# Optimization experiments

Measured on AMD Instinct MI355X. Metric: run time of the kernel, lower is better.

Reference implementation:

```python
import math
import jax
import jax.numpy as jnp
import numpy as np

N_NODE = 50000
N_EDGE = 1_600_000
D_IN = 128
D_K = 32
N_HEADS = 8


def setup_inputs() -> dict:
    key = jax.random.key(0)
    k_h, k_e, k_q, k_k, k_v = jax.random.split(key, 5)
    h = jax.random.normal(k_h, (N_NODE, D_IN), dtype=jnp.float32)
    edge_idx = jax.random.randint(k_e, (2, N_EDGE), 0, N_NODE, dtype=jnp.int64)
    scale = 1.0 / math.sqrt(D_IN)
    WQ = jax.random.normal(k_q, (N_HEADS, D_IN, D_K), dtype=jnp.float32) * scale
    WK = jax.random.normal(k_k, (N_HEADS, D_IN, D_K), dtype=jnp.float32) * scale
    WV = jax.random.normal(k_v, (N_HEADS, D_IN, D_K), dtype=jnp.float32) * scale
    return {"h": h, "edge_idx": edge_idx, "WQ": WQ, "WK": WK, "WV": WV}


def reference(h, edge_idx, WQ, WK, WV):
    n_node = h.shape[0]
    d_k = WK.shape[-1]
    # Per-head projections: [H, N, d]
    Q = jnp.einsum('nd,hdk->hnk', h, WQ)
    K = jnp.einsum('nd,hdk->hnk', h, WK)
    V = jnp.einsum('nd,hdv->hnv', h, WV)
    row = edge_idx[0]  # destination (softmax normalized per row, dim=1)
    col = edge_idx[1]  # source
    # Edge logits: e[h, e] = <Q[h, row[e]], K[h, col[e]]> / sqrt(d_k)
    e = jnp.einsum('hek,hek->he', Q[:, row, :], K[:, col, :]) / jnp.sqrt(
        jnp.asarray(d_k, dtype=h.dtype))
    eT = e.T  # [E, H]
    # Sparse (segment) softmax over outgoing edges of each row node.
    m = jax.ops.segment_max(eT, row, num_segments=n_node)  # [N, H]
    m = jnp.where(jnp.isfinite(m), m, jnp.zeros_like(m))   # guard empty rows
    ex = jnp.exp(eT - m[row])                               # [E, H]
    denom = jax.ops.segment_sum(ex, row, num_segments=n_node)  # [N, H]
    att = ex / denom[row]                                   # [E, H]
    # Sparse mm: out[i] = sum_{edges (i,j)} att * V[j]
    msgs = att[:, :, None] * jnp.transpose(V, (1, 0, 2))[col]  # [E, H, d_v]
    out = jax.ops.segment_sum(msgs, row, num_segments=n_node)  # [N, H, d_v]
    # aggregate == 'concat' -> head-major concat along feature dim
    return out.reshape(n_node, -1)
```

## Files before the change

kernel.cpp:

```cpp
#include <hip/hip_runtime.h>
#include <hip/hip_bf16.h>
#include <cstdint>

#define D_IN 128
#define DK 32
#define NH 8
#define HD 256

typedef __attribute__((ext_vector_type(8))) short short8;
typedef __attribute__((ext_vector_type(4))) float f32x4;

__device__ inline float u2f(unsigned int u) {
  union { unsigned int i; float f; } c; c.i = u; return c.f;
}
__device__ inline short f2bf(float f) {
  union { float f; unsigned int i; } c; c.f = f;
  unsigned int u = c.i;
  u = u + 0x7FFFu + ((u >> 16) & 1u);
  return (short)(u >> 16);
}

__global__ __launch_bounds__(256) void prep_w_kernel(
    const float* __restrict__ WQ, const float* __restrict__ WK,
    const float* __restrict__ WV, short8* __restrict__ Bbuf) {
  int ct = blockIdx.x;
  int t = threadIdx.x;
  int kt = t >> 6, L = t & 63;
  int col = ct * 16 + (L & 15);
  int type = col >> 8;
  const float* W = (type == 0) ? WQ : (type == 1) ? WK : WV;
  int head = (col & 255) >> 5;
  int kk = col & 31;
  int k0 = kt * 32 + ((L >> 4) << 3);
  short8 o;
  #pragma unroll
  for (int r = 0; r < 8; r++)
    o[r] = f2bf(W[head * (D_IN * DK) + (k0 + r) * DK + kk]);
  Bbuf[(size_t)(ct * 4 + kt) * 64 + L] = o;
}

__global__ __launch_bounds__(256) void gemm_qkv_kernel(
    const float* __restrict__ h, const short8* __restrict__ Bbuf,
    __hip_bfloat16* __restrict__ Qh, __hip_bfloat16* __restrict__ KVh,
    int nt_total, int n_node) {
  __shared__ float hs[16][132];
  __shared__ short lds[16][768];
  int nt = blockIdx.x;
  int t = threadIdx.x;
  {
    const float4* h4 = (const float4*)(h + (size_t)nt * 16 * 128);
    float4 v0 = h4[t * 2], v1 = h4[t * 2 + 1];
    int node = t >> 4, dim = (t & 15) * 8;
    hs[node][dim + 0] = v0.x; hs[node][dim + 1] = v0.y;
    hs[node][dim + 2] = v0.z; hs[node][dim + 3] = v0.w;
    hs[node][dim + 4] = v1.x; hs[node][dim + 5] = v1.y;
    hs[node][dim + 6] = v1.z; hs[node][dim + 7] = v1.w;
  }
  __syncthreads();
  int w = t >> 6;
  int L = t & 63;
  int arow = L & 15, k0base = ((L >> 4) << 3);
  short8 afrag[4];
  #pragma unroll
  for (int kt = 0; kt < 4; kt++) {
    #pragma unroll
    for (int r = 0; r < 8; r++)
      afrag[kt][r] = f2bf(hs[arow][kt * 32 + k0base + r]);
  }
  f32x4 acc[12];
  #pragma unroll
  for (int c = 0; c < 12; c++) acc[c] = (f32x4){0.f, 0.f, 0.f, 0.f};
  #pragma unroll
  for (int kt = 0; kt < 4; kt++) {
    #pragma unroll
    for (int c = 0; c < 12; c++) {
      short8 b = Bbuf[(size_t)((w * 12 + c) * 4 + kt) * 64 + L];
      acc[c] = __builtin_amdgcn_mfma_f32_16x16x32_bf16(afrag[kt], b, acc[c], 0, 0, 0);
    }
  }
  int row0 = (L >> 4) << 2;
  int col0 = w * 192 + (L & 15);
  #pragma unroll
  for (int c = 0; c < 12; c++) {
    #pragma unroll
    for (int r = 0; r < 4; r++)
      lds[row0 + r][col0 + c * 16] = f2bf(acc[c][r]);
  }
  __syncthreads();
  #pragma unroll
  for (int j = 0; j < 2; j++) {
    int u = t + j * 256;
    int hh = u >> 6, r2 = (u >> 2) & 15, part = u & 3;
    float4 vdat = *(const float4*)&lds[r2][hh * 32 + part * 8];
    *(float4*)(Qh + ((size_t)hh * n_node + nt * 16 + r2) * 32 + part * 8) = vdat;
  }
  #pragma unroll
  for (int j = 0; j < 4; j++) {
    int u = t + j * 256;
    int hh = u >> 7, r2 = (u >> 3) & 15, part = u & 7;
    int srccol = (part < 4) ? (256 + hh * 32 + part * 8)
                            : (512 + hh * 32 + (part - 4) * 8);
    float4 vdat = *(const float4*)&lds[r2][srccol];
    *(float4*)(KVh + ((size_t)hh * n_node + nt * 16 + r2) * 64 +
               ((part < 4) ? part * 8 : 32 + (part - 4) * 8)) = vdat;
  }
}

__global__ void rank_kernel(const int* __restrict__ row, int n_edge,
                            int* __restrict__ cnt, int* __restrict__ rank) {
  int i = blockIdx.x * blockDim.x + threadIdx.x;
  if (i < n_edge) rank[i] = atomicAdd(&cnt[row[i]], 1);
}

__global__ __launch_bounds__(256) void scan1_kernel(
    const int* __restrict__ cnt, int n, int* __restrict__ exc,
    int* __restrict__ bsum) {
  __shared__ int s[256];
  int gid = blockIdx.x * 256 + threadIdx.x;
  int v = (gid < n) ? cnt[gid] : 0;
  s[threadIdx.x] = v;
  __syncthreads();
  #pragma unroll
  for (int off = 1; off < 256; off <<= 1) {
    int t = (threadIdx.x >= off) ? s[threadIdx.x - off] : 0;
    __syncthreads();
    s[threadIdx.x] += t;
    __syncthreads();
  }
  if (gid < n) exc[gid] = s[threadIdx.x] - v;
  if (threadIdx.x == 255) bsum[blockIdx.x] = s[255];
}

__global__ __launch_bounds__(256) void scan2_kernel(int* __restrict__ bsum,
                                                    int nb) {
  __shared__ int s[256];
  int v = (threadIdx.x < nb) ? bsum[threadIdx.x] : 0;
  s[threadIdx.x] = v;
  __syncthreads();
  #pragma unroll
  for (int off = 1; off < 256; off <<= 1) {
    int t = (threadIdx.x >= off) ? s[threadIdx.x - off] : 0;
    __syncthreads();
    s[threadIdx.x] += t;
    __syncthreads();
  }
  if (threadIdx.x < nb) bsum[threadIdx.x] = s[threadIdx.x] - v;
}

__global__ __launch_bounds__(256) void scan3_kernel(
    int* __restrict__ exc, const int* __restrict__ bsum, int n, int n_edge) {
  int gid = blockIdx.x * 256 + threadIdx.x;
  if (gid < n) exc[gid] = exc[gid] + bsum[blockIdx.x];
  if (gid == 0) exc[n] = n_edge;
}

__global__ void scatter_kernel(const int* __restrict__ row,
                               const int* __restrict__ col,
                               const int* __restrict__ rank, int n_edge,
                               const int* __restrict__ offsets,
                               int* __restrict__ col_sorted) {
  int i = blockIdx.x * blockDim.x + threadIdx.x;
  if (i < n_edge) col_sorted[offsets[row[i]] + rank[i]] = col[i];
}

#define PROC(r, vld)                                                         \
  {                                                                          \
    float x0 = u2f(r.x << 16), x1 = u2f(r.x & 0xFFFF0000u);                  \
    float x2 = u2f(r.y << 16), x3 = u2f(r.y & 0xFFFF0000u);                  \
    float x4 = u2f(r.z << 16), x5 = u2f(r.z & 0xFFFF0000u);                  \
    float x6 = u2f(r.w << 16), x7 = u2f(r.w & 0xFFFF0000u);                  \
    float d = x0 * qf0;                                                      \
    d = fmaf(x1, qf1, d); d = fmaf(x2, qf2, d); d = fmaf(x3, qf3, d);        \
    d = fmaf(x4, qf4, d); d = fmaf(x5, qf5, d); d = fmaf(x6, qf6, d);        \
    d = fmaf(x7, qf7, d);                                                    \
    d += __shfl_xor(d, 1);                                                   \
    d += __shfl_xor(d, 2);                                                   \
    float tt = __shfl_xor(d, 4);                                             \
    float lg = (s < 4) ? d : tt;                                             \
    float p = (vld) ? __expf(lg) : 0.f;                                      \
    denom += p;                                                              \
    a0 = fmaf(p, x0, a0); a1 = fmaf(p, x1, a1);                              \
    a2 = fmaf(p, x2, a2); a3 = fmaf(p, x3, a3);                              \
    a4 = fmaf(p, x4, a4); a5 = fmaf(p, x5, a5);                              \
    a6 = fmaf(p, x6, a6); a7 = fmaf(p, x7, a7);                              \
  }

__global__ __launch_bounds__(256) void attn_kernel(
    const __hip_bfloat16* __restrict__ Qh, const __hip_bfloat16* __restrict__ KVh,
    const int* __restrict__ offsets, const int* __restrict__ col_sorted,
    float* __restrict__ out, int n_node) {
  int head = blockIdx.x & 7;
  int grp = blockIdx.x >> 3;
  int wave = threadIdx.x >> 6;
  int lane = threadIdx.x & 63;
  int g = lane >> 3;
  int s = lane & 7;
  int node = grp * 4 + wave;
  if (node >= n_node) return;
  int start = offsets[node], end = offsets[node + 1];

  if (end <= start) {
    if (g == 0 && s >= 4) {
      float* op = out + (size_t)node * HD + head * 32 + (s - 4) * 8;
      float4 z = make_float4(0.f, 0.f, 0.f, 0.f);
      *(float4*)op = z;
      *(float4*)(op + 4) = z;
    }
    return;
  }

  const float QS = 0.17677669529663687f;
  float qf0, qf1, qf2, qf3, qf4, qf5, qf6, qf7;
  {
    uint4 qr = *(const uint4*)((const char*)(Qh +
                ((size_t)head * n_node + node) * 32) + (s & 3) * 16);
    qf0 = u2f(qr.x << 16) * QS; qf1 = u2f(qr.x & 0xFFFF0000u) * QS;
    qf2 = u2f(qr.y << 16) * QS; qf3 = u2f(qr.y & 0xFFFF0000u) * QS;
    qf4 = u2f(qr.z << 16) * QS; qf5 = u2f(qr.z & 0xFFFF0000u) * QS;
    qf6 = u2f(qr.w << 16) * QS; qf7 = u2f(qr.w & 0xFFFF0000u) * QS;
  }
  float denom = 0.f;
  float a0 = 0.f, a1 = 0.f, a2 = 0.f, a3 = 0.f;
  float a4 = 0.f, a5 = 0.f, a6 = 0.f, a7 = 0.f;

  const char* kvb = (const char*)KVh + (size_t)head * n_node * 128 + s * 16;

  for (int base = start; base < end; base += 16) {
    int i0 = base + g, i1 = base + 8 + g;
    bool v0 = i0 < end, v1 = i1 < end;
    int c0 = col_sorted[v0 ? i0 : start];
    int c1 = col_sorted[v1 ? i1 : start];
    uint4 r0 = *(const uint4*)(kvb + (size_t)c0 * 128);
    uint4 r1 = *(const uint4*)(kvb + (size_t)c1 * 128);
    PROC(r0, v0);
    PROC(r1, v1);
  }

  denom += __shfl_xor(denom, 8); denom += __shfl_xor(denom, 16);
  denom += __shfl_xor(denom, 32);
  a0 += __shfl_xor(a0, 8); a0 += __shfl_xor(a0, 16); a0 += __shfl_xor(a0, 32);
  a1 += __shfl_xor(a1, 8); a1 += __shfl_xor(a1, 16); a1 += __shfl_xor(a1, 32);
  a2 += __shfl_xor(a2, 8); a2 += __shfl_xor(a2, 16); a2 += __shfl_xor(a2, 32);
  a3 += __shfl_xor(a3, 8); a3 += __shfl_xor(a3, 16); a3 += __shfl_xor(a3, 32);
  a4 += __shfl_xor(a4, 8); a4 += __shfl_xor(a4, 16); a4 += __shfl_xor(a4, 32);
  a5 += __shfl_xor(a5, 8); a5 += __shfl_xor(a5, 16); a5 += __shfl_xor(a5, 32);
  a6 += __shfl_xor(a6, 8); a6 += __shfl_xor(a6, 16); a6 += __shfl_xor(a6, 32);
  a7 += __shfl_xor(a7, 8); a7 += __shfl_xor(a7, 16); a7 += __shfl_xor(a7, 32);

  float inv = 1.f / denom;
  if (g == 0 && s >= 4) {
    float* op = out + (size_t)node * HD + head * 32 + (s - 4) * 8;
    float4 o0 = make_float4(a0 * inv, a1 * inv, a2 * inv, a3 * inv);
    float4 o1 = make_float4(a4 * inv, a5 * inv, a6 * inv, a7 * inv);
    *(float4*)op = o0;
    *(float4*)(op + 4) = o1;
  }
}

extern "C" void kernel_launch(void* const* d_in, const int* in_sizes, int n_in,
                              void* d_out, int out_size, void* d_ws,
                              size_t ws_size, hipStream_t stream) {
  const float* h = (const float*)d_in[0];
  const int* edge = (const int*)d_in[1];
  const float* WQ = (const float*)d_in[2];
  const float* WK = (const float*)d_in[3];
  const float* WV = (const float*)d_in[4];
  float* out = (float*)d_out;

  int n_node = in_sizes[0] / D_IN;
  int n_edge = in_sizes[1] / 2;
  const int* row = edge;
  const int* col = edge + n_edge;

  char* ws = (char*)d_ws;
  size_t off = 0;
  auto alloc = [&](size_t bytes) {
    void* p = ws + off;
    off += (bytes + 255) & ~(size_t)255;
    return p;
  };
  int nt_total = (n_node + 15) / 16;
  __hip_bfloat16* Qh = (__hip_bfloat16*)alloc((size_t)NH * n_node * 32 * 2);
  __hip_bfloat16* KVh = (__hip_bfloat16*)alloc((size_t)NH * n_node * 64 * 2);
  short8* Bbuf = (short8*)alloc((size_t)48 * 4 * 64 * 16);
  int* col_sorted = (int*)alloc((size_t)n_edge * 4);
  int* rank = (int*)alloc((size_t)n_edge * 4);
  int* cnt = (int*)alloc((size_t)n_node * 4);
  int* offsets = (int*)alloc((size_t)(n_node + 1) * 4);
  int* bsum = (int*)alloc(256 * 4);

  hipMemsetAsync(cnt, 0, (size_t)n_node * 4, stream);

  prep_w_kernel<<<48, 256, 0, stream>>>(WQ, WK, WV, Bbuf);
  gemm_qkv_kernel<<<nt_total, 256, 0, stream>>>(h, Bbuf, Qh, KVh, nt_total,
                                                n_node);

  int nb_e = (n_edge + 255) / 256;
  rank_kernel<<<nb_e, 256, 0, stream>>>(row, n_edge, cnt, rank);

  int nb = (n_node + 255) / 256;
  scan1_kernel<<<nb, 256, 0, stream>>>(cnt, n_node, offsets, bsum);
  scan2_kernel<<<1, 256, 0, stream>>>(bsum, nb);
  scan3_kernel<<<nb, 256, 0, stream>>>(offsets, bsum, n_node, n_edge);

  scatter_kernel<<<nb_e, 256, 0, stream>>>(row, col, rank, n_edge, offsets,
                                           col_sorted);

  attn_kernel<<<((n_node + 3) / 4) * 8, 256, 0, stream>>>(
      Qh, KVh, offsets, col_sorted, out, n_node);
}
```

Baseline: 368.4 us.

## Compute edge logits with MFMA and fold softmax scale into Q projection

The per-edge Q·K dot products in the attention kernel now come from a 16x16x32 bf16 MFMA over 16 gathered K rows, instead of scalar FMAs followed by shuffle reductions. The 1/sqrt(d_k)·log2(e) factor is applied to Q when it is written out in the projection kernel, so the attention loop can use exp2f directly. K and V gathers are split across lanes in a new layout, and the final reduction needs fewer shuffles. This removes shuffle and ALU work per edge, at the cost of separate K and V gathers per lane and a select to pick each lane's weight. The softmax still has no max subtraction, as before.

```diff
diff --git a/kernel.cpp b/kernel.cpp
--- a/kernel.cpp
+++ b/kernel.cpp
@@ -80,11 +80,13 @@
   }
   int row0 = (L >> 4) << 2;
   int col0 = w * 192 + (L & 15);
+  const float QSL = 0.25506966f;
   #pragma unroll
   for (int c = 0; c < 12; c++) {
+    float sc = ((w * 192 + c * 16) < 256) ? QSL : 1.f;
     #pragma unroll
     for (int r = 0; r < 4; r++)
-      lds[row0 + r][col0 + c * 16] = f2bf(acc[c][r]);
+      lds[row0 + r][col0 + c * 16] = f2bf(acc[c][r] * sc);
   }
   __syncthreads();
   #pragma unroll
@@ -163,45 +165,27 @@
   if (i < n_edge) col_sorted[offsets[row[i]] + rank[i]] = col[i];
 }
 
-#define PROC(r, vld)                                                         \
-  {                                                                          \
-    float x0 = u2f(r.x << 16), x1 = u2f(r.x & 0xFFFF0000u);                  \
-    float x2 = u2f(r.y << 16), x3 = u2f(r.y & 0xFFFF0000u);                  \
-    float x4 = u2f(r.z << 16), x5 = u2f(r.z & 0xFFFF0000u);                  \
-    float x6 = u2f(r.w << 16), x7 = u2f(r.w & 0xFFFF0000u);                  \
-    float d = x0 * qf0;                                                      \
-    d = fmaf(x1, qf1, d); d = fmaf(x2, qf2, d); d = fmaf(x3, qf3, d);        \
-    d = fmaf(x4, qf4, d); d = fmaf(x5, qf5, d); d = fmaf(x6, qf6, d);        \
-    d = fmaf(x7, qf7, d);                                                    \
-    d += __shfl_xor(d, 1);                                                   \
-    d += __shfl_xor(d, 2);                                                   \
-    float tt = __shfl_xor(d, 4);                                             \
-    float lg = (s < 4) ? d : tt;                                             \
-    float p = (vld) ? __expf(lg) : 0.f;                                      \
-    denom += p;                                                              \
-    a0 = fmaf(p, x0, a0); a1 = fmaf(p, x1, a1);                              \
-    a2 = fmaf(p, x2, a2); a3 = fmaf(p, x3, a3);                              \
-    a4 = fmaf(p, x4, a4); a5 = fmaf(p, x5, a5);                              \
-    a6 = fmaf(p, x6, a6); a7 = fmaf(p, x7, a7);                              \
-  }
-
 __global__ __launch_bounds__(256) void attn_kernel(
     const __hip_bfloat16* __restrict__ Qh, const __hip_bfloat16* __restrict__ KVh,
     const int* __restrict__ offsets, const int* __restrict__ col_sorted,
     float* __restrict__ out, int n_node) {
   int head = blockIdx.x & 7;
   int grp = blockIdx.x >> 3;
-  int wave = threadIdx.x >> 6;
+  int wv = threadIdx.x >> 6;
   int lane = threadIdx.x & 63;
-  int g = lane >> 3;
-  int s = lane & 7;
-  int node = grp * 4 + wave;
+  int node = grp * 4 + wv;
   if (node >= n_node) return;
   int start = offsets[node], end = offsets[node + 1];
 
+  int kc = lane >> 4;
+  int erow = lane & 15;
+  int vc = lane & 3;
+  int vchunk = (lane >> 2) & 3;
+  int vslot = (kc << 2) | vc;
+
   if (end <= start) {
-    if (g == 0 && s >= 4) {
-      float* op = out + (size_t)node * HD + head * 32 + (s - 4) * 8;
+    if (vc == 0 && kc == 0) {
+      float* op = out + (size_t)node * HD + head * 32 + vchunk * 8;
       float4 z = make_float4(0.f, 0.f, 0.f, 0.f);
       *(float4*)op = z;
       *(float4*)(op + 4) = z;
@@ -209,47 +193,48 @@
     return;
   }
 
-  const float QS = 0.17677669529663687f;
-  float qf0, qf1, qf2, qf3, qf4, qf5, qf6, qf7;
-  {
-    uint4 qr = *(const uint4*)((const char*)(Qh +
-                ((size_t)head * n_node + node) * 32) + (s & 3) * 16);
-    qf0 = u2f(qr.x << 16) * QS; qf1 = u2f(qr.x & 0xFFFF0000u) * QS;
-    qf2 = u2f(qr.y << 16) * QS; qf3 = u2f(qr.y & 0xFFFF0000u) * QS;
-    qf4 = u2f(qr.z << 16) * QS; qf5 = u2f(qr.z & 0xFFFF0000u) * QS;
-    qf6 = u2f(qr.w << 16) * QS; qf7 = u2f(qr.w & 0xFFFF0000u) * QS;
-  }
-  float denom = 0.f;
+  short8 qb = *(const short8*)(Qh + ((size_t)head * n_node + node) * 32 + kc * 8);
+
+  float dn = 0.f;
   float a0 = 0.f, a1 = 0.f, a2 = 0.f, a3 = 0.f;
   float a4 = 0.f, a5 = 0.f, a6 = 0.f, a7 = 0.f;
-
-  const char* kvb = (const char*)KVh + (size_t)head * n_node * 128 + s * 16;
+  const char* kvb = (const char*)KVh + (size_t)head * n_node * 128;
 
   for (int base = start; base < end; base += 16) {
-    int i0 = base + g, i1 = base + 8 + g;
-    bool v0 = i0 < end, v1 = i1 < end;
-    int c0 = col_sorted[v0 ? i0 : start];
-    int c1 = col_sorted[v1 ? i1 : start];
-    uint4 r0 = *(const uint4*)(kvb + (size_t)c0 * 128);
-    uint4 r1 = *(const uint4*)(kvb + (size_t)c1 * 128);
-    PROC(r0, v0);
-    PROC(r1, v1);
-  }
-
-  denom += __shfl_xor(denom, 8); denom += __shfl_xor(denom, 16);
-  denom += __shfl_xor(denom, 32);
-  a0 += __shfl_xor(a0, 8); a0 += __shfl_xor(a0, 16); a0 += __shfl_xor(a0, 32);
-  a1 += __shfl_xor(a1, 8); a1 += __shfl_xor(a1, 16); a1 += __shfl_xor(a1, 32);
-  a2 += __shfl_xor(a2, 8); a2 += __shfl_xor(a2, 16); a2 += __shfl_xor(a2, 32);
-  a3 += __shfl_xor(a3, 8); a3 += __shfl_xor(a3, 16); a3 += __shfl_xor(a3, 32);
-  a4 += __shfl_xor(a4, 8); a4 += __shfl_xor(a4, 16); a4 += __shfl_xor(a4, 32);
-  a5 += __shfl_xor(a5, 8); a5 += __shfl_xor(a5, 16); a5 += __shfl_xor(a5, 32);
-  a6 += __shfl_xor(a6, 8); a6 += __shfl_xor(a6, 16); a6 += __shfl_xor(a6, 32);
-  a7 += __shfl_xor(a7, 8); a7 += __shfl_xor(a7, 16); a7 += __shfl_xor(a7, 32);
-
-  float inv = 1.f / denom;
-  if (g == 0 && s >= 4) {
-    float* op = out + (size_t)node * HD + head * 32 + (s - 4) * 8;
+    int iK = base + erow;
+    int iV = base + vslot;
+    int cK = col_sorted[iK < end ? iK : start];
+    int cV = col_sorted[iV < end ? iV : start];
+    short8 kf = *(const short8*)(kvb + (size_t)cK * 128 + kc * 16);
+    uint4 vf = *(const uint4*)(kvb + (size_t)cV * 128 + 64 + vchunk * 16);
+    f32x4 dm = __builtin_amdgcn_mfma_f32_16x16x32_bf16(
+        kf, qb, (f32x4){0.f, 0.f, 0.f, 0.f}, 0, 0, 0);
+    int e0 = base + (kc << 2);
+    float p0 = (e0 < end) ? exp2f(dm[0]) : 0.f;
+    float p1 = (e0 + 1 < end) ? exp2f(dm[1]) : 0.f;
+    float p2 = (e0 + 2 < end) ? exp2f(dm[2]) : 0.f;
+    float p3 = (e0 + 3 < end) ? exp2f(dm[3]) : 0.f;
+    dn += (p0 + p1) + (p2 + p3);
+    float pb = (vc == 0) ? p0 : (vc == 1) ? p1 : (vc == 2) ? p2 : p3;
+    a0 = fmaf(pb, u2f(vf.x << 16), a0);
+    a1 = fmaf(pb, u2f(vf.x & 0xFFFF0000u), a1);
+    a2 = fmaf(pb, u2f(vf.y << 16), a2);
+    a3 = fmaf(pb, u2f(vf.y & 0xFFFF0000u), a3);
+    a4 = fmaf(pb, u2f(vf.z << 16), a4);
+    a5 = fmaf(pb, u2f(vf.z & 0xFFFF0000u), a5);
+    a6 = fmaf(pb, u2f(vf.w << 16), a6);
+    a7 = fmaf(pb, u2f(vf.w & 0xFFFF0000u), a7);
+  }
+
+#define RED4(x)                                                              \
+  x += __shfl_xor(x, 1); x += __shfl_xor(x, 2);                              \
+  x += __shfl_xor(x, 16); x += __shfl_xor(x, 32);
+  RED4(a0) RED4(a1) RED4(a2) RED4(a3) RED4(a4) RED4(a5) RED4(a6) RED4(a7)
+  dn += __shfl_xor(dn, 16);
+  dn += __shfl_xor(dn, 32);
+  float inv = 1.f / dn;
+  if (vc == 0 && kc == 0) {
+    float* op = out + (size_t)node * HD + head * 32 + vchunk * 8;
     float4 o0 = make_float4(a0 * inv, a1 * inv, a2 * inv, a3 * inv);
     float4 o1 = make_float4(a4 * inv, a5 * inv, a6 * inv, a7 * inv);
     *(float4*)op = o0;
```

Result: slower. 454.1 us (+23.3%).

## Pad CSR rows to multiples of 16 with a zero sentinel node, drop bounds checks

Applied to the files above, without the earlier changes.

Each node's edge segment is padded to a multiple of 16 and filled with a sentinel column that points to an extra all-zero K/V row. This removes the per-edge validity predicates in the attention loop. Each padded edge contributes exp(0)=1 to the denominator, which is subtracted using the true count. The Q scale is folded into the GEMM as 1/sqrt(d)*log2(e) so the loop can use exp2f. The cost is a fill kernel over the padded column array, a larger col_sorted buffer, and extra wasted gathers of the zero row. Like the original code, it skips the max subtraction and depends on the logits staying small.

```diff
diff --git a/kernel.cpp b/kernel.cpp
--- a/kernel.cpp
+++ b/kernel.cpp
@@ -80,11 +80,13 @@
   }
   int row0 = (L >> 4) << 2;
   int col0 = w * 192 + (L & 15);
+  const float QSL = 0.25506966f;
   #pragma unroll
   for (int c = 0; c < 12; c++) {
+    float sc = ((w * 192 + c * 16) < 256) ? QSL : 1.f;
     #pragma unroll
     for (int r = 0; r < 4; r++)
-      lds[row0 + r][col0 + c * 16] = f2bf(acc[c][r]);
+      lds[row0 + r][col0 + c * 16] = f2bf(acc[c][r] * sc);
   }
   __syncthreads();
   #pragma unroll
@@ -101,8 +103,18 @@
     int srccol = (part < 4) ? (256 + hh * 32 + part * 8)
                             : (512 + hh * 32 + (part - 4) * 8);
     float4 vdat = *(const float4*)&lds[r2][srccol];
-    *(float4*)(KVh + ((size_t)hh * n_node + nt * 16 + r2) * 64 +
+    *(float4*)(KVh + ((size_t)hh * (n_node + 1) + nt * 16 + r2) * 64 +
                ((part < 4) ? part * 8 : 32 + (part - 4) * 8)) = vdat;
+  }
+}
+
+__global__ void fill_kernel(int* __restrict__ col_sorted, int cap,
+                            __hip_bfloat16* __restrict__ KVh, int n_node) {
+  int i = blockIdx.x * 256 + threadIdx.x;
+  if (i < cap) col_sorted[i] = n_node;
+  if (i < 512) {
+    int hh = i >> 6, j = i & 63;
+    KVh[((size_t)hh * (n_node + 1) + n_node) * 64 + j] = __float2bfloat16(0.f);
   }
 }
 
@@ -117,7 +129,7 @@
     int* __restrict__ bsum) {
   __shared__ int s[256];
   int gid = blockIdx.x * 256 + threadIdx.x;
-  int v = (gid < n) ? cnt[gid] : 0;
+  int v = (gid < n) ? ((cnt[gid] + 15) & ~15) : 0;
   s[threadIdx.x] = v;
   __syncthreads();
   #pragma unroll
@@ -148,10 +160,14 @@
 }
 
 __global__ __launch_bounds__(256) void scan3_kernel(
-    int* __restrict__ exc, const int* __restrict__ bsum, int n, int n_edge) {
+    int* __restrict__ exc, const int* __restrict__ bsum,
+    const int* __restrict__ cnt, int n) {
   int gid = blockIdx.x * 256 + threadIdx.x;
-  if (gid < n) exc[gid] = exc[gid] + bsum[blockIdx.x];
-  if (gid == 0) exc[n] = n_edge;
+  if (gid < n) {
+    int o = exc[gid] + bsum[blockIdx.x];
+    exc[gid] = o;
+    if (gid == n - 1) exc[n] = o + ((cnt[gid] + 15) & ~15);
+  }
 }
 
 __global__ void scatter_kernel(const int* __restrict__ row,
@@ -163,7 +179,7 @@
   if (i < n_edge) col_sorted[offsets[row[i]] + rank[i]] = col[i];
 }
 
-#define PROC(r, vld)                                                         \
+#define PROC(r)                                                              \
   {                                                                          \
     float x0 = u2f(r.x << 16), x1 = u2f(r.x & 0xFFFF0000u);                  \
     float x2 = u2f(r.y << 16), x3 = u2f(r.y & 0xFFFF0000u);                  \
@@ -177,8 +193,8 @@
     d += __shfl_xor(d, 2);                                                   \
     float tt = __shfl_xor(d, 4);                                             \
     float lg = (s < 4) ? d : tt;                                             \
-    float p = (vld) ? __expf(lg) : 0.f;                                      \
-    denom += p;                                                              \
+    float p = exp2f(lg);                                                     \
+    dn += p;                                                                 \
     a0 = fmaf(p, x0, a0); a1 = fmaf(p, x1, a1);                              \
     a2 = fmaf(p, x2, a2); a3 = fmaf(p, x3, a3);                              \
     a4 = fmaf(p, x4, a4); a5 = fmaf(p, x5, a5);                              \
@@ -187,15 +203,15 @@
 
 __global__ __launch_bounds__(256) void attn_kernel(
     const __hip_bfloat16* __restrict__ Qh, const __hip_bfloat16* __restrict__ KVh,
-    const int* __restrict__ offsets, const int* __restrict__ col_sorted,
-    float* __restrict__ out, int n_node) {
+    const int* __restrict__ offsets, const int* __restrict__ cnt,
+    const int* __restrict__ col_sorted, float* __restrict__ out, int n_node) {
   int head = blockIdx.x & 7;
   int grp = blockIdx.x >> 3;
-  int wave = threadIdx.x >> 6;
+  int wv = threadIdx.x >> 6;
   int lane = threadIdx.x & 63;
   int g = lane >> 3;
   int s = lane & 7;
-  int node = grp * 4 + wave;
+  int node = grp * 4 + wv;
   if (node >= n_node) return;
   int start = offsets[node], end = offsets[node + 1];
 
@@ -209,35 +225,31 @@
     return;
   }
 
-  const float QS = 0.17677669529663687f;
   float qf0, qf1, qf2, qf3, qf4, qf5, qf6, qf7;
   {
     uint4 qr = *(const uint4*)((const char*)(Qh +
                 ((size_t)head * n_node + node) * 32) + (s & 3) * 16);
-    qf0 = u2f(qr.x << 16) * QS; qf1 = u2f(qr.x & 0xFFFF0000u) * QS;
-    qf2 = u2f(qr.y << 16) * QS; qf3 = u2f(qr.y & 0xFFFF0000u) * QS;
-    qf4 = u2f(qr.z << 16) * QS; qf5 = u2f(qr.z & 0xFFFF0000u) * QS;
-    qf6 = u2f(qr.w << 16) * QS; qf7 = u2f(qr.w & 0xFFFF0000u) * QS;
-  }
-  float denom = 0.f;
+    qf0 = u2f(qr.x << 16); qf1 = u2f(qr.x & 0xFFFF0000u);
+    qf2 = u2f(qr.y << 16); qf3 = u2f(qr.y & 0xFFFF0000u);
+    qf4 = u2f(qr.z << 16); qf5 = u2f(qr.z & 0xFFFF0000u);
+    qf6 = u2f(qr.w << 16); qf7 = u2f(qr.w & 0xFFFF0000u);
+  }
+  float dn = 0.f;
   float a0 = 0.f, a1 = 0.f, a2 = 0.f, a3 = 0.f;
   float a4 = 0.f, a5 = 0.f, a6 = 0.f, a7 = 0.f;
 
-  const char* kvb = (const char*)KVh + (size_t)head * n_node * 128 + s * 16;
+  const char* kvb = (const char*)KVh + (size_t)head * (n_node + 1) * 128 + s * 16;
 
   for (int base = start; base < end; base += 16) {
-    int i0 = base + g, i1 = base + 8 + g;
-    bool v0 = i0 < end, v1 = i1 < end;
-    int c0 = col_sorted[v0 ? i0 : start];
-    int c1 = col_sorted[v1 ? i1 : start];
+    int c0 = col_sorted[base + g];
+    int c1 = col_sorted[base + 8 + g];
     uint4 r0 = *(const uint4*)(kvb + (size_t)c0 * 128);
     uint4 r1 = *(const uint4*)(kvb + (size_t)c1 * 128);
-    PROC(r0, v0);
-    PROC(r1, v1);
-  }
-
-  denom += __shfl_xor(denom, 8); denom += __shfl_xor(denom, 16);
-  denom += __shfl_xor(denom, 32);
+    PROC(r0);
+    PROC(r1);
+  }
+
+  dn += __shfl_xor(dn, 8); dn += __shfl_xor(dn, 16); dn += __shfl_xor(dn, 32);
   a0 += __shfl_xor(a0, 8); a0 += __shfl_xor(a0, 16); a0 += __shfl_xor(a0, 32);
   a1 += __shfl_xor(a1, 8); a1 += __shfl_xor(a1, 16); a1 += __shfl_xor(a1, 32);
   a2 += __shfl_xor(a2, 8); a2 += __shfl_xor(a2, 16); a2 += __shfl_xor(a2, 32);
@@ -247,7 +259,8 @@
   a6 += __shfl_xor(a6, 8); a6 += __shfl_xor(a6, 16); a6 += __shfl_xor(a6, 32);
   a7 += __shfl_xor(a7, 8); a7 += __shfl_xor(a7, 16); a7 += __shfl_xor(a7, 32);
 
-  float inv = 1.f / denom;
+  dn -= (float)((end - start) - cnt[node]);
+  float inv = 1.f / dn;
   if (g == 0 && s >= 4) {
     float* op = out + (size_t)node * HD + head * 32 + (s - 4) * 8;
     float4 o0 = make_float4(a0 * inv, a1 * inv, a2 * inv, a3 * inv);
@@ -280,10 +293,11 @@
     return p;
   };
   int nt_total = (n_node + 15) / 16;
+  int cap = n_edge + 15 * n_node;
   __hip_bfloat16* Qh = (__hip_bfloat16*)alloc((size_t)NH * n_node * 32 * 2);
-  __hip_bfloat16* KVh = (__hip_bfloat16*)alloc((size_t)NH * n_node * 64 * 2);
+  __hip_bfloat16* KVh = (__hip_bfloat16*)alloc((size_t)NH * (n_node + 1) * 64 * 2);
   short8* Bbuf = (short8*)alloc((size_t)48 * 4 * 64 * 16);
-  int* col_sorted = (int*)alloc((size_t)n_edge * 4);
+  int* col_sorted = (int*)alloc((size_t)cap * 4);
   int* rank = (int*)alloc((size_t)n_edge * 4);
   int* cnt = (int*)alloc((size_t)n_node * 4);
   int* offsets = (int*)alloc((size_t)(n_node + 1) * 4);
@@ -294,6 +308,8 @@
   prep_w_kernel<<<48, 256, 0, stream>>>(WQ, WK, WV, Bbuf);
   gemm_qkv_kernel<<<nt_total, 256, 0, stream>>>(h, Bbuf, Qh, KVh, nt_total,
                                                 n_node);
+  fill_kernel<<<(cap + 255) / 256, 256, 0, stream>>>(col_sorted, cap, KVh,
+                                                     n_node);
 
   int nb_e = (n_edge + 255) / 256;
   rank_kernel<<<nb_e, 256, 0, stream>>>(row, n_edge, cnt, rank);
@@ -301,11 +317,11 @@
   int nb = (n_node + 255) / 256;
   scan1_kernel<<<nb, 256, 0, stream>>>(cnt, n_node, offsets, bsum);
   scan2_kernel<<<1, 256, 0, stream>>>(bsum, nb);
-  scan3_kernel<<<nb, 256, 0, stream>>>(offsets, bsum, n_node, n_edge);
+  scan3_kernel<<<nb, 256, 0, stream>>>(offsets, bsum, cnt, n_node);
 
   scatter_kernel<<<nb_e, 256, 0, stream>>>(row, col, rank, n_edge, offsets,
                                            col_sorted);
 
   attn_kernel<<<((n_node + 3) / 4) * 8, 256, 0, stream>>>(
-      Qh, KVh, offsets, col_sorted, out, n_node);
-}
+      Qh, KVh, offsets, cnt, col_sorted, out, n_node);
+}
```

After: 376.7 us. +2.3%, slower.
